# Kernel optimization log

Measured on AMD Instinct MI355X. Metric: run time of the kernel, lower is better.

Reference implementation:

```python
import jax, jax.numpy as jnp
import numpy as np
import math

D_MODEL, D_K, D_V = 1024, 64, 64
B, S = 4, 4096


def setup_inputs() -> dict:
    key = jax.random.key(0)
    ks = jax.random.split(key, 7)
    lim = 1.0 / math.sqrt(D_MODEL)
    return {
        "embeddings": jax.random.normal(ks[0], (B, S, D_MODEL), dtype=jnp.float32),
        "Wq": jax.random.uniform(ks[1], (D_MODEL, D_K), minval=-lim, maxval=lim, dtype=jnp.float32),
        "bq": jax.random.uniform(ks[2], (D_K,), minval=-lim, maxval=lim, dtype=jnp.float32),
        "Wk": jax.random.uniform(ks[3], (D_MODEL, D_K), minval=-lim, maxval=lim, dtype=jnp.float32),
        "bk": jax.random.uniform(ks[4], (D_K,), minval=-lim, maxval=lim, dtype=jnp.float32),
        "Wv": jax.random.uniform(ks[5], (D_MODEL, D_V), minval=-lim, maxval=lim, dtype=jnp.float32),
        "bv": jax.random.uniform(ks[6], (D_V,), minval=-lim, maxval=lim, dtype=jnp.float32),
    }


def reference(embeddings, Wq, bq, Wk, bk, Wv, bv):
    # Q, K: [B, S, d_k]; V: [B, S, d_v]
    Q = embeddings @ Wq + bq
    K = embeddings @ Wk + bk
    V = embeddings @ Wv + bv
    scale = 1.0 / math.sqrt(D_K)
    # scores: [B, S, S]
    scores = jnp.einsum("bsk,btk->bst", Q, K) * scale
    attn = jax.nn.softmax(scores, axis=-1)
    return jnp.einsum("bst,btv->bsv", attn, V)
```

## Files before the change

kernel.cpp:

```cpp
#include <hip/hip_runtime.h>

#define SEQ  4096
#define DMODEL 1024
#define QTOT 16384
#define NQK (QTOT * 128)
#define NV  (QTOT * 64)

typedef __bf16 bf16x8 __attribute__((ext_vector_type(8)));
typedef unsigned short u16x8 __attribute__((ext_vector_type(8)));
typedef float f32x4 __attribute__((ext_vector_type(4)));

static __device__ __forceinline__ unsigned short f2bfbits(float f) {
    unsigned int u = __builtin_bit_cast(unsigned int, f);
    unsigned int lsb = (u >> 16) & 1u;
    u += 0x7fffu + lsb;
    return (unsigned short)(u >> 16);
}

static __device__ __forceinline__ bf16x8 ld_frag(const unsigned short* p) {
    uint4 u = *reinterpret_cast<const uint4*>(p);
    return __builtin_bit_cast(bf16x8, u);
}

static __device__ __forceinline__ void stp(float* p, float v) { *p = v; }
static __device__ __forceinline__ void stp(unsigned short* p, float v) { *p = f2bfbits(v); }

__global__ void prep_weights(const float* __restrict__ Wq,
                             const float* __restrict__ Wk,
                             const float* __restrict__ Wv,
                             unsigned short* __restrict__ WtS) {
    int o = blockIdx.x * 256 + threadIdx.x;
    int f = o >> 9, q = o & 511;
    int lane = q >> 3, j = q & 7;
    int kc = f / 12, nt = f - kc * 12;
    int n = nt * 16 + (lane & 15);
    int k = kc * 32 + (lane >> 4) * 8 + j;
    float v;
    if (n < 64)       v = Wq[k * 64 + n];
    else if (n < 128) v = Wk[k * 64 + (n - 64)];
    else              v = Wv[k * 64 + (n - 128)];
    WtS[o] = f2bfbits(v);
}

template <typename T>
__global__ __launch_bounds__(256) void proj_split(
        const float* __restrict__ emb, const unsigned short* __restrict__ WtS,
        T* __restrict__ PQK, T* __restrict__ PV) {
    const int tid = threadIdx.x;
    const int w = tid >> 6, lane = tid & 63;
    const int c = lane & 15, qd = lane >> 4;
    const int split = blockIdx.x >> 8;
    const int tb = blockIdx.x & 255;
    const int mbase = tb * 64 + w * 16;
    const int kbase = split * 512;

    f32x4 acc[12];
#pragma unroll
    for (int i = 0; i < 12; i++) acc[i] = (f32x4){0.f, 0.f, 0.f, 0.f};

    const float* ap = emb + (size_t)(mbase + c) * DMODEL + kbase + qd * 8;
    const unsigned short* wp = WtS + (size_t)(kbase >> 5) * 6144 + lane * 8;

    float4 e0a = *reinterpret_cast<const float4*>(ap);
    float4 e0b = *reinterpret_cast<const float4*>(ap + 4);
    float4 e1a = *reinterpret_cast<const float4*>(ap + 32);
    float4 e1b = *reinterpret_cast<const float4*>(ap + 36);
    bf16x8 wc[12];
#pragma unroll
    for (int nt = 0; nt < 12; nt++) wc[nt] = ld_frag(wp + nt * 512);

#pragma unroll
    for (int s = 0; s < 16; s++) {
        bf16x8 wn[12];
        if (s < 15) {
#pragma unroll
            for (int nt = 0; nt < 12; nt++)
                wn[nt] = ld_frag(wp + (s + 1) * 6144 + nt * 512);
        } else {
#pragma unroll
            for (int nt = 0; nt < 12; nt++) wn[nt] = wc[nt];
        }
        float4 e2a, e2b;
        if (s < 14) {
            e2a = *reinterpret_cast<const float4*>(ap + (s + 2) * 32);
            e2b = *reinterpret_cast<const float4*>(ap + (s + 2) * 32 + 4);
        } else { e2a = e1a; e2b = e1b; }

        u16x8 at;
        at[0] = f2bfbits(e0a.x); at[1] = f2bfbits(e0a.y);
        at[2] = f2bfbits(e0a.z); at[3] = f2bfbits(e0a.w);
        at[4] = f2bfbits(e0b.x); at[5] = f2bfbits(e0b.y);
        at[6] = f2bfbits(e0b.z); at[7] = f2bfbits(e0b.w);
        bf16x8 af = __builtin_bit_cast(bf16x8, at);

#pragma unroll
        for (int nt = 0; nt < 12; nt++)
            acc[nt] = __builtin_amdgcn_mfma_f32_16x16x32_bf16(af, wc[nt], acc[nt], 0, 0, 0);

        e0a = e1a; e0b = e1b; e1a = e2a; e1b = e2b;
#pragma unroll
        for (int nt = 0; nt < 12; nt++) wc[nt] = wn[nt];
    }

#pragma unroll
    for (int nt = 0; nt < 12; nt++) {
        int n = nt * 16 + c;
#pragma unroll
        for (int r = 0; r < 4; r++) {
            int token = mbase + qd * 4 + r;
            if (n < 128)
                stp(&PQK[(size_t)split * NQK + (size_t)token * 128 + n], acc[nt][r]);
            else {
                int bb = token >> 12, s = token & 4095, v = n - 128;
                stp(&PV[(size_t)split * NV + ((size_t)bb << 18) + (v << 12) + s], acc[nt][r]);
            }
        }
    }
}

template <typename T>
__global__ __launch_bounds__(256) void merge_proj(
        const T* __restrict__ PQK, const T* __restrict__ PV,
        const float* __restrict__ bq, const float* __restrict__ bk,
        const float* __restrict__ bv,
        unsigned short* __restrict__ Qb, unsigned short* __restrict__ Kb,
        unsigned short* __restrict__ VT) {
    int idx4 = (blockIdx.x * 256 + threadIdx.x) * 4;
    float s[4];
    if (idx4 < NQK) {
        int token = idx4 >> 7, n = idx4 & 127;
#pragma unroll
        for (int j = 0; j < 4; j++) s[j] = 0.f;
#pragma unroll
        for (int kz = 0; kz < 2; kz++) {
            if constexpr (sizeof(T) == 4) {
                float4 v = *reinterpret_cast<const float4*>(&PQK[(size_t)kz * NQK + idx4]);
                s[0] += v.x; s[1] += v.y; s[2] += v.z; s[3] += v.w;
            } else {
                ushort4 v = *reinterpret_cast<const ushort4*>(&PQK[(size_t)kz * NQK + idx4]);
                s[0] += __builtin_bit_cast(float, (unsigned int)v.x << 16);
                s[1] += __builtin_bit_cast(float, (unsigned int)v.y << 16);
                s[2] += __builtin_bit_cast(float, (unsigned int)v.z << 16);
                s[3] += __builtin_bit_cast(float, (unsigned int)v.w << 16);
            }
        }
        const float* bias = (n < 64) ? bq + n : bk + (n - 64);
        unsigned short* dst = (n < 64) ? Qb + (size_t)token * 64 + n
                                       : Kb + (size_t)token * 64 + (n - 64);
#pragma unroll
        for (int j = 0; j < 4; j++) dst[j] = f2bfbits(s[j] + bias[j]);
    } else {
        int j0 = idx4 - NQK;
        int v = (j0 >> 12) & 63;
        float bias = bv[v];
#pragma unroll
        for (int j = 0; j < 4; j++) s[j] = bias;
#pragma unroll
        for (int kz = 0; kz < 2; kz++) {
            if constexpr (sizeof(T) == 4) {
                float4 vv = *reinterpret_cast<const float4*>(&PV[(size_t)kz * NV + j0]);
                s[0] += vv.x; s[1] += vv.y; s[2] += vv.z; s[3] += vv.w;
            } else {
                ushort4 vv = *reinterpret_cast<const ushort4*>(&PV[(size_t)kz * NV + j0]);
                s[0] += __builtin_bit_cast(float, (unsigned int)vv.x << 16);
                s[1] += __builtin_bit_cast(float, (unsigned int)vv.y << 16);
                s[2] += __builtin_bit_cast(float, (unsigned int)vv.z << 16);
                s[3] += __builtin_bit_cast(float, (unsigned int)vv.w << 16);
            }
        }
#pragma unroll
        for (int j = 0; j < 4; j++) VT[j0 + j] = f2bfbits(s[j]);
    }
}

__global__ __launch_bounds__(256) void proj_direct(
        const float* __restrict__ emb, const unsigned short* __restrict__ WtS,
        const float* __restrict__ bq, const float* __restrict__ bk,
        const float* __restrict__ bv,
        unsigned short* __restrict__ Qb, unsigned short* __restrict__ Kb,
        unsigned short* __restrict__ VT) {
    const int tid = threadIdx.x;
    const int w = tid >> 6, lane = tid & 63;
    const int c = lane & 15, qd = lane >> 4;
    const int mbase = blockIdx.x * 64 + w * 16;

    f32x4 acc[12];
#pragma unroll
    for (int i = 0; i < 12; i++) acc[i] = (f32x4){0.f, 0.f, 0.f, 0.f};

    const float* ap = emb + (size_t)(mbase + c) * DMODEL + qd * 8;
    const unsigned short* wp = WtS + lane * 8;

    float4 e0a = *reinterpret_cast<const float4*>(ap);
    float4 e0b = *reinterpret_cast<const float4*>(ap + 4);
    float4 e1a = *reinterpret_cast<const float4*>(ap + 32);
    float4 e1b = *reinterpret_cast<const float4*>(ap + 36);
    bf16x8 wc[12];
#pragma unroll
    for (int nt = 0; nt < 12; nt++) wc[nt] = ld_frag(wp + nt * 512);

#pragma unroll 4
    for (int s = 0; s < 32; s++) {
        bf16x8 wn[12];
        if (s < 31) {
#pragma unroll
            for (int nt = 0; nt < 12; nt++)
                wn[nt] = ld_frag(wp + (s + 1) * 6144 + nt * 512);
        } else {
#pragma unroll
            for (int nt = 0; nt < 12; nt++) wn[nt] = wc[nt];
        }
        float4 e2a, e2b;
        if (s < 30) {
            e2a = *reinterpret_cast<const float4*>(ap + (s + 2) * 32);
            e2b = *reinterpret_cast<const float4*>(ap + (s + 2) * 32 + 4);
        } else { e2a = e1a; e2b = e1b; }

        u16x8 at;
        at[0] = f2bfbits(e0a.x); at[1] = f2bfbits(e0a.y);
        at[2] = f2bfbits(e0a.z); at[3] = f2bfbits(e0a.w);
        at[4] = f2bfbits(e0b.x); at[5] = f2bfbits(e0b.y);
        at[6] = f2bfbits(e0b.z); at[7] = f2bfbits(e0b.w);
        bf16x8 af = __builtin_bit_cast(bf16x8, at);

#pragma unroll
        for (int nt = 0; nt < 12; nt++)
            acc[nt] = __builtin_amdgcn_mfma_f32_16x16x32_bf16(af, wc[nt], acc[nt], 0, 0, 0);

        e0a = e1a; e0b = e1b; e1a = e2a; e1b = e2b;
#pragma unroll
        for (int nt = 0; nt < 12; nt++) wc[nt] = wn[nt];
    }

#pragma unroll
    for (int nt = 0; nt < 12; nt++) {
        int n = nt * 16 + c;
        float bias = (n < 64) ? bq[n] : (n < 128) ? bk[n - 64] : bv[n - 128];
#pragma unroll
        for (int r = 0; r < 4; r++) {
            int token = mbase + qd * 4 + r;
            unsigned short bits = f2bfbits(acc[nt][r] + bias);
            if (n < 64)        Qb[(size_t)token * 64 + n] = bits;
            else if (n < 128)  Kb[(size_t)token * 64 + (n - 64)] = bits;
            else {
                int bb = token >> 12, ss = token & 4095;
                VT[((size_t)bb * 64 + (n - 128)) * SEQ + ss] = bits;
            }
        }
    }
}

__global__ __launch_bounds__(256) void attn(
        const unsigned short* __restrict__ Qb, const unsigned short* __restrict__ Kb,
        const unsigned short* __restrict__ VT,
        float* __restrict__ accP, float* __restrict__ lP,
        float* __restrict__ outDirect, int tlen, int gshift) {
    __shared__ __align__(16) unsigned short Kt[64 * 72];
    __shared__ __align__(16) unsigned short Vt[64 * 72];
    __shared__ __align__(16) unsigned short Pl[4][16 * 72];

    const int tid = threadIdx.x;
    const int w = tid >> 6, lane = tid & 63;
    const int c = lane & 15, qd = lane >> 4;
    const int g = blockIdx.x & ((1 << gshift) - 1);
    const int qblk = blockIdx.x >> gshift;
    const int split = g >> 2, b = g & 3;
    const int qbase = qblk * 64 + w * 16;
    const int tstart = split * tlen;
    const float kLS = 0.18033688011112042f;

    const unsigned short* Qp = Qb + ((size_t)(b << 12) + qbase + c) * 64 + qd * 8;
    bf16x8 aq0 = ld_frag(Qp);
    bf16x8 aq1 = ld_frag(Qp + 32);

    f32x4 acc[4];
#pragma unroll
    for (int i = 0; i < 4; i++) acc[i] = (f32x4){0.f, 0.f, 0.f, 0.f};
    float l_r[4] = {0.f, 0.f, 0.f, 0.f};

    for (int t0 = tstart; t0 < tstart + tlen; t0 += 64) {
        __syncthreads();
#pragma unroll
        for (int i = 0; i < 2; i++) {
            int ch = tid + 256 * i;
            int tr = ch >> 3, koff = (ch & 7) * 8;
            *reinterpret_cast<uint4*>(&Kt[tr * 72 + koff]) =
                *reinterpret_cast<const uint4*>(Kb + ((size_t)(b << 12) + t0 + tr) * 64 + koff);
            *reinterpret_cast<uint4*>(&Vt[tr * 72 + koff]) =
                *reinterpret_cast<const uint4*>(VT + ((size_t)b * 64 + tr) * SEQ + t0 + koff);
        }
        __syncthreads();

        f32x4 s[4];
#pragma unroll
        for (int ts = 0; ts < 4; ts++) {
            bf16x8 bk0 = ld_frag(&Kt[(ts * 16 + c) * 72 + qd * 8]);
            bf16x8 bk1 = ld_frag(&Kt[(ts * 16 + c) * 72 + 32 + qd * 8]);
            f32x4 z = (f32x4){0.f, 0.f, 0.f, 0.f};
            z = __builtin_amdgcn_mfma_f32_16x16x32_bf16(aq0, bk0, z, 0, 0, 0);
            z = __builtin_amdgcn_mfma_f32_16x16x32_bf16(aq1, bk1, z, 0, 0, 0);
            s[ts] = z;
        }

        float pv[4][4];
#pragma unroll
        for (int ts = 0; ts < 4; ts++)
#pragma unroll
            for (int r = 0; r < 4; r++)
                pv[ts][r] = __builtin_amdgcn_exp2f(s[ts][r] * kLS);
#pragma unroll
        for (int r = 0; r < 4; r++)
            l_r[r] += pv[0][r] + pv[1][r] + pv[2][r] + pv[3][r];

#pragma unroll
        for (int ts = 0; ts < 4; ts++)
#pragma unroll
            for (int r = 0; r < 4; r++)
                Pl[w][(qd * 4 + r) * 72 + ts * 16 + c] = f2bfbits(pv[ts][r]);

        bf16x8 ap0 = ld_frag(&Pl[w][c * 72 + qd * 8]);
        bf16x8 ap1 = ld_frag(&Pl[w][c * 72 + 32 + qd * 8]);
#pragma unroll
        for (int nt = 0; nt < 4; nt++) {
            bf16x8 bv0 = ld_frag(&Vt[(nt * 16 + c) * 72 + qd * 8]);
            bf16x8 bv1 = ld_frag(&Vt[(nt * 16 + c) * 72 + 32 + qd * 8]);
            acc[nt] = __builtin_amdgcn_mfma_f32_16x16x32_bf16(ap0, bv0, acc[nt], 0, 0, 0);
            acc[nt] = __builtin_amdgcn_mfma_f32_16x16x32_bf16(ap1, bv1, acc[nt], 0, 0, 0);
        }
    }

#pragma unroll
    for (int off = 1; off < 16; off <<= 1)
#pragma unroll
        for (int r = 0; r < 4; r++) l_r[r] += __shfl_xor(l_r[r], off);

    if (outDirect) {
#pragma unroll
        for (int nt = 0; nt < 4; nt++)
#pragma unroll
            for (int r = 0; r < 4; r++) {
                int q = qbase + qd * 4 + r;
                outDirect[(((size_t)b << 12) + q) * 64 + nt * 16 + c] = acc[nt][r] / l_r[r];
            }
    } else {
#pragma unroll
        for (int nt = 0; nt < 4; nt++)
#pragma unroll
            for (int r = 0; r < 4; r++) {
                size_t q = (size_t)(b << 12) + qbase + qd * 4 + r;
                accP[((size_t)split * QTOT + q) * 64 + nt * 16 + c] = acc[nt][r];
            }
        if (c == 0) {
#pragma unroll
            for (int r = 0; r < 4; r++)
                lP[(size_t)split * QTOT + (b << 12) + qbase + qd * 4 + r] = l_r[r];
        }
    }
}

__global__ __launch_bounds__(256) void merge_out(
        const float* __restrict__ accP, const float* __restrict__ lP,
        float* __restrict__ out, int ns) {
    int idx = blockIdx.x * 256 + threadIdx.x;
    int q = idx >> 6;
    float a = 0.f, l = 0.f;
    for (int s = 0; s < ns; s++) {
        a += accP[(size_t)s * QTOT * 64 + idx];
        l += lP[(size_t)s * QTOT + q];
    }
    out[idx] = a / l;
}

extern "C" void kernel_launch(void* const* d_in, const int* in_sizes, int n_in,
                              void* d_out, int out_size, void* d_ws, size_t ws_size,
                              hipStream_t stream) {
    const float* emb = (const float*)d_in[0];
    const float* Wq  = (const float*)d_in[1];
    const float* bq  = (const float*)d_in[2];
    const float* Wk  = (const float*)d_in[3];
    const float* bk  = (const float*)d_in[4];
    const float* Wv  = (const float*)d_in[5];
    const float* bv  = (const float*)d_in[6];
    float* out = (float*)d_out;

    unsigned short* ws = (unsigned short*)d_ws;
    unsigned short* WtS = ws;
    unsigned short* Qb = ws + 192 * 1024;
    unsigned short* Kb = Qb + QTOT * 64;
    unsigned short* VT = Kb + QTOT * 64;
    char* region = (char*)(VT + QTOT * 64);
    size_t avail = (ws_size > 6684672) ? ws_size - 6684672 : 0;

    int projMode = (avail >= (size_t)2 * (NQK + NV) * 4) ? 2
                 : (avail >= (size_t)2 * (NQK + NV) * 2) ? 1 : 0;
    size_t per = (size_t)QTOT * 64 * 4 + (size_t)QTOT * 4;
    int ns = (avail >= 4 * per) ? 4 : (avail >= 2 * per) ? 2 : (avail >= per) ? 1 : 0;

    prep_weights<<<768, 256, 0, stream>>>(Wq, Wk, Wv, WtS);

    if (projMode == 2) {
        float* PQKp = (float*)region;
        float* PVp  = PQKp + (size_t)2 * NQK;
        proj_split<float><<<512, 256, 0, stream>>>(emb, WtS, PQKp, PVp);
        merge_proj<float><<<3072, 256, 0, stream>>>(PQKp, PVp, bq, bk, bv, Qb, Kb, VT);
    } else if (projMode == 1) {
        unsigned short* PQKp = (unsigned short*)region;
        unsigned short* PVp  = PQKp + (size_t)2 * NQK;
        proj_split<unsigned short><<<512, 256, 0, stream>>>(emb, WtS, PQKp, PVp);
        merge_proj<unsigned short><<<3072, 256, 0, stream>>>(PQKp, PVp, bq, bk, bv, Qb, Kb, VT);
    } else {
        proj_direct<<<256, 256, 0, stream>>>(emb, WtS, bq, bk, bv, Qb, Kb, VT);
    }

    if (ns > 0) {
        float* accP = (float*)region;
        float* lP   = accP + (size_t)ns * QTOT * 64;
        int gshift = (ns == 4) ? 4 : (ns == 2) ? 3 : 2;
        attn<<<256 * ns, 256, 0, stream>>>(Qb, Kb, VT, accP, lP, nullptr, SEQ / ns, gshift);
        merge_out<<<(QTOT * 64) / 256, 256, 0, stream>>>(accP, lP, out, ns);
    } else {
        attn<<<256, 256, 0, stream>>>(Qb, Kb, VT, nullptr, nullptr, out, SEQ, 2);
    }
}
```

Baseline: 182.5 us.

## Restructure attention into key-split waves with in-block reduction and fold scale into Q

The attention kernel is rewritten so each 512-thread block handles 64 queries for one batch, and each of its 8 waves covers a 512-key slice. K and V fragments are read straight from global memory rather than staged through shared memory. Partial outputs are reduced across waves in shared memory, which replaces the separate split-K merge kernel and its global partial buffers. The softmax scale is folded into Q during projection, so the per-score multiply goes away. The trade-offs are higher register pressure from 16 accumulators, a grid of only 256 blocks, and synchronisation cost in the tree reduction.

```diff
diff --git a/kernel.cpp b/kernel.cpp
--- a/kernel.cpp
+++ b/kernel.cpp
@@ -5,6 +5,7 @@
 #define QTOT 16384
 #define NQK (QTOT * 128)
 #define NV  (QTOT * 64)
+#define QSCALE 0.18033688011112042f
 
 typedef __bf16 bf16x8 __attribute__((ext_vector_type(8)));
 typedef unsigned short u16x8 __attribute__((ext_vector_type(8)));
@@ -144,11 +145,13 @@
                 s[3] += __builtin_bit_cast(float, (unsigned int)v.w << 16);
             }
         }
-        const float* bias = (n < 64) ? bq + n : bk + (n - 64);
-        unsigned short* dst = (n < 64) ? Qb + (size_t)token * 64 + n
-                                       : Kb + (size_t)token * 64 + (n - 64);
-#pragma unroll
-        for (int j = 0; j < 4; j++) dst[j] = f2bfbits(s[j] + bias[j]);
+        bool isQ = (n < 64);
+        const float* bias = isQ ? bq + n : bk + (n - 64);
+        float fac = isQ ? QSCALE : 1.0f;
+        unsigned short* dst = isQ ? Qb + (size_t)token * 64 + n
+                                  : Kb + (size_t)token * 64 + (n - 64);
+#pragma unroll
+        for (int j = 0; j < 4; j++) dst[j] = f2bfbits((s[j] + bias[j]) * fac);
     } else {
         int j0 = idx4 - NQK;
         int v = (j0 >> 12) & 63;
@@ -236,10 +239,11 @@
     for (int nt = 0; nt < 12; nt++) {
         int n = nt * 16 + c;
         float bias = (n < 64) ? bq[n] : (n < 128) ? bk[n - 64] : bv[n - 128];
+        float fac = (n < 64) ? QSCALE : 1.0f;
 #pragma unroll
         for (int r = 0; r < 4; r++) {
             int token = mbase + qd * 4 + r;
-            unsigned short bits = f2bfbits(acc[nt][r] + bias);
+            unsigned short bits = f2bfbits((acc[nt][r] + bias) * fac);
             if (n < 64)        Qb[(size_t)token * 64 + n] = bits;
             else if (n < 128)  Kb[(size_t)token * 64 + (n - 64)] = bits;
             else {
@@ -250,125 +254,157 @@
     }
 }
 
-__global__ __launch_bounds__(256) void attn(
+__global__ __launch_bounds__(512, 2) void attn(
         const unsigned short* __restrict__ Qb, const unsigned short* __restrict__ Kb,
-        const unsigned short* __restrict__ VT,
-        float* __restrict__ accP, float* __restrict__ lP,
-        float* __restrict__ outDirect, int tlen, int gshift) {
-    __shared__ __align__(16) unsigned short Kt[64 * 72];
-    __shared__ __align__(16) unsigned short Vt[64 * 72];
-    __shared__ __align__(16) unsigned short Pl[4][16 * 72];
+        const unsigned short* __restrict__ VT, float* __restrict__ out) {
+    __shared__ __align__(16) unsigned short Pl[8][64 * 72];
+    __shared__ float l_all[8][64];
 
     const int tid = threadIdx.x;
     const int w = tid >> 6, lane = tid & 63;
     const int c = lane & 15, qd = lane >> 4;
-    const int g = blockIdx.x & ((1 << gshift) - 1);
-    const int qblk = blockIdx.x >> gshift;
-    const int split = g >> 2, b = g & 3;
-    const int qbase = qblk * 64 + w * 16;
-    const int tstart = split * tlen;
-    const float kLS = 0.18033688011112042f;
-
-    const unsigned short* Qp = Qb + ((size_t)(b << 12) + qbase + c) * 64 + qd * 8;
-    bf16x8 aq0 = ld_frag(Qp);
-    bf16x8 aq1 = ld_frag(Qp + 32);
-
-    f32x4 acc[4];
-#pragma unroll
-    for (int i = 0; i < 4; i++) acc[i] = (f32x4){0.f, 0.f, 0.f, 0.f};
-    float l_r[4] = {0.f, 0.f, 0.f, 0.f};
-
-    for (int t0 = tstart; t0 < tstart + tlen; t0 += 64) {
-        __syncthreads();
-#pragma unroll
-        for (int i = 0; i < 2; i++) {
-            int ch = tid + 256 * i;
-            int tr = ch >> 3, koff = (ch & 7) * 8;
-            *reinterpret_cast<uint4*>(&Kt[tr * 72 + koff]) =
-                *reinterpret_cast<const uint4*>(Kb + ((size_t)(b << 12) + t0 + tr) * 64 + koff);
-            *reinterpret_cast<uint4*>(&Vt[tr * 72 + koff]) =
-                *reinterpret_cast<const uint4*>(VT + ((size_t)b * 64 + tr) * SEQ + t0 + koff);
-        }
-        __syncthreads();
-
-        f32x4 s[4];
+    const int g3 = blockIdx.x & 7;
+    const int b = g3 >> 1;
+    const int qblk = ((blockIdx.x >> 3) << 1) | (g3 & 1);
+    const int qbase = qblk * 64;
+    const int tstart = w * 512;
+
+    bf16x8 aq0[4], aq1[4];
+#pragma unroll
+    for (int qs = 0; qs < 4; qs++) {
+        const unsigned short* Qp = Qb + ((size_t)(b << 12) + qbase + qs * 16 + c) * 64 + qd * 8;
+        aq0[qs] = ld_frag(Qp);
+        aq1[qs] = ld_frag(Qp + 32);
+    }
+
+    f32x4 acc[16];
+#pragma unroll
+    for (int i = 0; i < 16; i++) acc[i] = (f32x4){0.f, 0.f, 0.f, 0.f};
+    float lsum[4][4];
+#pragma unroll
+    for (int qs = 0; qs < 4; qs++)
+#pragma unroll
+        for (int r = 0; r < 4; r++) lsum[qs][r] = 0.f;
+
+    unsigned short* myP = &Pl[w][0];
+
+#pragma unroll 2
+    for (int it = 0; it < 8; it++) {
+        const int t0 = tstart + it * 64;
+        const unsigned short* Kt = Kb + ((size_t)(b << 12) + t0) * 64;
+
+        bf16x8 bk0[4], bk1[4];
 #pragma unroll
         for (int ts = 0; ts < 4; ts++) {
-            bf16x8 bk0 = ld_frag(&Kt[(ts * 16 + c) * 72 + qd * 8]);
-            bf16x8 bk1 = ld_frag(&Kt[(ts * 16 + c) * 72 + 32 + qd * 8]);
-            f32x4 z = (f32x4){0.f, 0.f, 0.f, 0.f};
-            z = __builtin_amdgcn_mfma_f32_16x16x32_bf16(aq0, bk0, z, 0, 0, 0);
-            z = __builtin_amdgcn_mfma_f32_16x16x32_bf16(aq1, bk1, z, 0, 0, 0);
-            s[ts] = z;
-        }
-
-        float pv[4][4];
-#pragma unroll
-        for (int ts = 0; ts < 4; ts++)
+            bk0[ts] = ld_frag(Kt + (ts * 16 + c) * 64 + qd * 8);
+            bk1[ts] = ld_frag(Kt + (ts * 16 + c) * 64 + 32 + qd * 8);
+        }
+
+#pragma unroll
+        for (int qs = 0; qs < 4; qs++) {
+            f32x4 sc[4];
+#pragma unroll
+            for (int ts = 0; ts < 4; ts++) {
+                f32x4 z = (f32x4){0.f, 0.f, 0.f, 0.f};
+                z = __builtin_amdgcn_mfma_f32_16x16x32_bf16(aq0[qs], bk0[ts], z, 0, 0, 0);
+                z = __builtin_amdgcn_mfma_f32_16x16x32_bf16(aq1[qs], bk1[ts], z, 0, 0, 0);
+                sc[ts] = z;
+            }
+#pragma unroll
+            for (int ts = 0; ts < 4; ts++)
+#pragma unroll
+                for (int r = 0; r < 4; r++) {
+                    float p = __builtin_amdgcn_exp2f(sc[ts][r]);
+                    lsum[qs][r] += p;
+                    myP[(qs * 16 + qd * 4 + r) * 72 + ts * 16 + c] = f2bfbits(p);
+                }
+        }
+
+        bf16x8 bv0[4], bv1[4];
+#pragma unroll
+        for (int nt = 0; nt < 4; nt++) {
+            const unsigned short* Vp = VT + (((size_t)b * 64 + nt * 16 + c) << 12) + t0 + qd * 8;
+            bv0[nt] = ld_frag(Vp);
+            bv1[nt] = ld_frag(Vp + 32);
+        }
+
+#pragma unroll
+        for (int qs = 0; qs < 4; qs++) {
+            bf16x8 ap0 = ld_frag(&myP[(qs * 16 + c) * 72 + qd * 8]);
+            bf16x8 ap1 = ld_frag(&myP[(qs * 16 + c) * 72 + 32 + qd * 8]);
+#pragma unroll
+            for (int nt = 0; nt < 4; nt++) {
+                acc[qs * 4 + nt] = __builtin_amdgcn_mfma_f32_16x16x32_bf16(ap0, bv0[nt], acc[qs * 4 + nt], 0, 0, 0);
+                acc[qs * 4 + nt] = __builtin_amdgcn_mfma_f32_16x16x32_bf16(ap1, bv1[nt], acc[qs * 4 + nt], 0, 0, 0);
+            }
+        }
+    }
+
+#pragma unroll
+    for (int off = 1; off < 16; off <<= 1)
+#pragma unroll
+        for (int qs = 0; qs < 4; qs++)
+#pragma unroll
+            for (int r = 0; r < 4; r++) lsum[qs][r] += __shfl_xor(lsum[qs][r], off);
+    if (c == 0) {
+#pragma unroll
+        for (int qs = 0; qs < 4; qs++)
 #pragma unroll
             for (int r = 0; r < 4; r++)
-                pv[ts][r] = __builtin_amdgcn_exp2f(s[ts][r] * kLS);
-#pragma unroll
-        for (int r = 0; r < 4; r++)
-            l_r[r] += pv[0][r] + pv[1][r] + pv[2][r] + pv[3][r];
-
-#pragma unroll
-        for (int ts = 0; ts < 4; ts++)
-#pragma unroll
-            for (int r = 0; r < 4; r++)
-                Pl[w][(qd * 4 + r) * 72 + ts * 16 + c] = f2bfbits(pv[ts][r]);
-
-        bf16x8 ap0 = ld_frag(&Pl[w][c * 72 + qd * 8]);
-        bf16x8 ap1 = ld_frag(&Pl[w][c * 72 + 32 + qd * 8]);
-#pragma unroll
-        for (int nt = 0; nt < 4; nt++) {
-            bf16x8 bv0 = ld_frag(&Vt[(nt * 16 + c) * 72 + qd * 8]);
-            bf16x8 bv1 = ld_frag(&Vt[(nt * 16 + c) * 72 + 32 + qd * 8]);
-            acc[nt] = __builtin_amdgcn_mfma_f32_16x16x32_bf16(ap0, bv0, acc[nt], 0, 0, 0);
-            acc[nt] = __builtin_amdgcn_mfma_f32_16x16x32_bf16(ap1, bv1, acc[nt], 0, 0, 0);
-        }
-    }
-
-#pragma unroll
-    for (int off = 1; off < 16; off <<= 1)
-#pragma unroll
-        for (int r = 0; r < 4; r++) l_r[r] += __shfl_xor(l_r[r], off);
-
-    if (outDirect) {
-#pragma unroll
-        for (int nt = 0; nt < 4; nt++)
+                l_all[w][qs * 16 + qd * 4 + r] = lsum[qs][r];
+    }
+
+    float* red = (float*)&Pl[0][0];
+    __syncthreads();
+    if (w >= 4) {
+        float* rp = red + (w - 4) * 4352 + lane * 68;
+#pragma unroll
+        for (int i = 0; i < 16; i++) *reinterpret_cast<f32x4*>(rp + i * 4) = acc[i];
+    }
+    __syncthreads();
+    if (w < 4) {
+        float* rp = red + w * 4352 + lane * 68;
+#pragma unroll
+        for (int i = 0; i < 16; i++) acc[i] += *reinterpret_cast<const f32x4*>(rp + i * 4);
+    }
+    __syncthreads();
+    if (w == 2 || w == 3) {
+        float* rp = red + (w - 2) * 4352 + lane * 68;
+#pragma unroll
+        for (int i = 0; i < 16; i++) *reinterpret_cast<f32x4*>(rp + i * 4) = acc[i];
+    }
+    __syncthreads();
+    if (w < 2) {
+        float* rp = red + w * 4352 + lane * 68;
+#pragma unroll
+        for (int i = 0; i < 16; i++) acc[i] += *reinterpret_cast<const f32x4*>(rp + i * 4);
+    }
+    __syncthreads();
+    if (w == 1) {
+        float* rp = red + lane * 68;
+#pragma unroll
+        for (int i = 0; i < 16; i++) *reinterpret_cast<f32x4*>(rp + i * 4) = acc[i];
+    }
+    __syncthreads();
+    if (w == 0) {
+        float* rp = red + lane * 68;
+#pragma unroll
+        for (int i = 0; i < 16; i++) acc[i] += *reinterpret_cast<const f32x4*>(rp + i * 4);
+#pragma unroll
+        for (int qs = 0; qs < 4; qs++)
 #pragma unroll
             for (int r = 0; r < 4; r++) {
-                int q = qbase + qd * 4 + r;
-                outDirect[(((size_t)b << 12) + q) * 64 + nt * 16 + c] = acc[nt][r] / l_r[r];
-            }
-    } else {
-#pragma unroll
-        for (int nt = 0; nt < 4; nt++)
-#pragma unroll
-            for (int r = 0; r < 4; r++) {
-                size_t q = (size_t)(b << 12) + qbase + qd * 4 + r;
-                accP[((size_t)split * QTOT + q) * 64 + nt * 16 + c] = acc[nt][r];
-            }
-        if (c == 0) {
-#pragma unroll
-            for (int r = 0; r < 4; r++)
-                lP[(size_t)split * QTOT + (b << 12) + qbase + qd * 4 + r] = l_r[r];
-        }
-    }
-}
-
-__global__ __launch_bounds__(256) void merge_out(
-        const float* __restrict__ accP, const float* __restrict__ lP,
-        float* __restrict__ out, int ns) {
-    int idx = blockIdx.x * 256 + threadIdx.x;
-    int q = idx >> 6;
-    float a = 0.f, l = 0.f;
-    for (int s = 0; s < ns; s++) {
-        a += accP[(size_t)s * QTOT * 64 + idx];
-        l += lP[(size_t)s * QTOT + q];
-    }
-    out[idx] = a / l;
+                int q = qs * 16 + qd * 4 + r;
+                float l = 0.f;
+#pragma unroll
+                for (int ww = 0; ww < 8; ww++) l += l_all[ww][q];
+                float inv = 1.0f / l;
+                size_t row = (size_t)(b << 12) + qbase + q;
+#pragma unroll
+                for (int nt = 0; nt < 4; nt++)
+                    out[row * 64 + nt * 16 + c] = acc[qs * 4 + nt][r] * inv;
+            }
+    }
 }
 
 extern "C" void kernel_launch(void* const* d_in, const int* in_sizes, int n_in,
@@ -393,8 +429,6 @@
 
     int projMode = (avail >= (size_t)2 * (NQK + NV) * 4) ? 2
                  : (avail >= (size_t)2 * (NQK + NV) * 2) ? 1 : 0;
-    size_t per = (size_t)QTOT * 64 * 4 + (size_t)QTOT * 4;
-    int ns = (avail >= 4 * per) ? 4 : (avail >= 2 * per) ? 2 : (avail >= per) ? 1 : 0;
 
     prep_weights<<<768, 256, 0, stream>>>(Wq, Wk, Wv, WtS);
 
@@ -412,13 +446,5 @@
         proj_direct<<<256, 256, 0, stream>>>(emb, WtS, bq, bk, bv, Qb, Kb, VT);
     }
 
-    if (ns > 0) {
-        float* accP = (float*)region;
-        float* lP   = accP + (size_t)ns * QTOT * 64;
-        int gshift = (ns == 4) ? 4 : (ns == 2) ? 3 : 2;
-        attn<<<256 * ns, 256, 0, stream>>>(Qb, Kb, VT, accP, lP, nullptr, SEQ / ns, gshift);
-        merge_out<<<(QTOT * 64) / 256, 256, 0, stream>>>(accP, lP, out, ns);
-    } else {
-        attn<<<256, 256, 0, stream>>>(Qb, Kb, VT, nullptr, nullptr, out, SEQ, 2);
-    }
-}
+    attn<<<256, 512, 0, stream>>>(Qb, Kb, VT, out);
+}
```

New measurement: 173.3 us. -5.1%, faster.
